# Kernel optimization log

Measured on AMD Instinct MI355X. Metric: run time of the kernel, lower is better.

## Reference

```python
import jax, jax.numpy as jnp
from jax import lax
import numpy as np

BN_EPS = 1e-3


def _bn_train(x, gamma, beta):
    # training-mode BatchNorm2d: batch stats over (N, H, W), biased variance
    mean = jnp.mean(x, axis=(0, 2, 3), keepdims=True)
    var = jnp.var(x, axis=(0, 2, 3), keepdims=True)
    g = gamma[None, :, None, None]
    b = beta[None, :, None, None]
    return (x - mean) * lax.rsqrt(var + BN_EPS) * g + b


def _pointwise(x, w, b, gamma, beta):
    # 1x1 conv + BN + relu (reluM = clamp(min=0))
    y = jnp.einsum('bchw,oc->bohw', x, w) + b[None, :, None, None]
    return jnp.maximum(_bn_train(y, gamma, beta), 0.0)


def _depthwise1d(x, w, b, gamma, beta):
    # depthwise (1,5) conv, zero pad width by 2 each side, BN, clamp(-8,8)
    C = w.shape[0]
    k = w[:, None, None, :]  # [C,1,1,5]
    y = lax.conv_general_dilated(
        x, k, window_strides=(1, 1), padding=[(0, 0), (2, 2)],
        feature_group_count=C,
        dimension_numbers=('NCHW', 'OIHW', 'NCHW'))
    y = y + b[None, :, None, None]
    return jnp.clip(_bn_train(y, gamma, beta), -8.0, 8.0)


def _iir(x, w3, gamma, beta):
    # y[0] = (a+b+c)*x[0];  y[r] = a*x[r] + b*x[r-1] + c*y[r-1]
    a = w3[0][:, None]  # w_curr_inp, [C,1]
    b = w3[1][:, None]  # w_prev_inp
    c = w3[2][:, None]  # w_prev_out
    xT = jnp.moveaxis(x, 2, 0)  # [H,B,C,W]
    y0 = (a + b + c) * xT[0]

    def step(y_prev, xs):
        x_curr, x_prev = xs
        y = a * x_curr + b * x_prev + c * y_prev
        return y, y

    _, ys = lax.scan(step, y0, (xT[1:], xT[:-1]))
    y = jnp.concatenate([y0[None], ys], axis=0)
    y = jnp.moveaxis(y, 0, 2)  # back to [B,C,H,W]
    return jnp.clip(_bn_train(y, gamma, beta), -8.0, 8.0)


def _process_unit(x, u, iir_w, iir_gamma, iir_beta, dw_w, dw_b, dw_gamma,
                  dw_beta, pw_w, pw_b, pw_gamma, pw_beta):
    h = _iir(x, iir_w[u], iir_gamma[u], iir_beta[u])
    h = _depthwise1d(h, dw_w[u], dw_b[u], dw_gamma[u], dw_beta[u])
    return _pointwise(h, pw_w[u], pw_b[u], pw_gamma[u], pw_beta[u])


def setup_inputs() -> dict:
    key = jax.random.key(0)
    ks = jax.random.split(key, 16)
    B, Cin, Cout, H, W = 4, 36, 72, 256, 256
    return {
        'x': jax.random.normal(ks[0], (B, Cin, H, W), jnp.float32),
        'expand_w': jax.random.normal(ks[1], (Cout, Cin), jnp.float32),
        'expand_b': jax.random.normal(ks[2], (Cout,), jnp.float32),
        'expand_gamma': jax.random.uniform(ks[3], (Cout,), jnp.float32),
        'expand_beta': jax.random.normal(ks[4], (Cout,), jnp.float32),
        'iir_w': jax.random.uniform(ks[5], (4, 3, Cout), jnp.float32),
        'iir_gamma': jax.random.uniform(ks[6], (4, Cout), jnp.float32),
        'iir_beta': jax.random.normal(ks[7], (4, Cout), jnp.float32),
        'dw_w': jax.random.normal(ks[8], (4, Cout, 5), jnp.float32),
        'dw_b': jax.random.normal(ks[9], (4, Cout), jnp.float32),
        'dw_gamma': jax.random.uniform(ks[10], (4, Cout), jnp.float32),
        'dw_beta': jax.random.normal(ks[11], (4, Cout), jnp.float32),
        'pw_w': jax.random.normal(ks[12], (4, Cout, Cout), jnp.float32),
        'pw_b': jax.random.normal(ks[13], (4, Cout), jnp.float32),
        'pw_gamma': jax.random.uniform(ks[14], (4, Cout), jnp.float32),
        'pw_beta': jax.random.normal(ks[15], (4, Cout), jnp.float32),
    }


def reference(x, expand_w, expand_b, expand_gamma, expand_beta, iir_w,
              iir_gamma, iir_beta, dw_w, dw_b, dw_gamma, dw_beta, pw_w,
              pw_b, pw_gamma, pw_beta):
    h = _pointwise(x, expand_w, expand_b, expand_gamma, expand_beta)
    unit = lambda z, u: _process_unit(z, u, iir_w, iir_gamma, iir_beta, dw_w,
                                      dw_b, dw_gamma, dw_beta, pw_w, pw_b,
                                      pw_gamma, pw_beta)
    h = h + unit(unit(h, 0), 1)
    h = h + unit(unit(h, 2), 3)
    return h
```

## Files before the change

### kernel.cpp

```cpp
#include <hip/hip_runtime.h>
#include <hip/hip_fp16.h>

#define BBATCH 4
#define CCH 72
#define HROW 256
#define WCOL 256
#define HWSZ (HROW*WCOL)
#define NPC (BBATCH*HROW*WCOL)
#define BNEPS 1e-3f
#define NSH 64
#define SST 144

typedef unsigned short u16;
typedef unsigned int u32;
typedef _Float16 h8 __attribute__((ext_vector_type(8)));
typedef float f32x4 __attribute__((ext_vector_type(4)));

__device__ __forceinline__ float h2f(u16 h_){ return __half2float(__ushort_as_half(h_)); }
__device__ __forceinline__ u16 f2h(float f){ return __half_as_ushort(__float2half(f)); }
__device__ __forceinline__ u32 pack2(float a, float b){ return (u32)f2h(a) | ((u32)f2h(b)<<16); }
__device__ __forceinline__ float clip8(float v){ return fminf(fmaxf(v,-8.f),8.f); }

__device__ __forceinline__ void get_ss_wave(int c, int lane, const float* __restrict__ pstat,
                                            const float* __restrict__ gam, const float* __restrict__ bet,
                                            float& sc, float& sh){
  float s = pstat[lane*SST + c];
  float q = pstat[lane*SST + 72 + c];
  #pragma unroll
  for (int off=32; off; off>>=1){ s += __shfl_xor(s,off); q += __shfl_xor(q,off); }
  float mean = s * (1.0f/(float)NPC);
  float var  = q * (1.0f/(float)NPC) - mean*mean;
  sc = gam[c] * rsqrtf(var + BNEPS);
  sh = bet[c] - mean*sc;
}

template<int CIN, int RAW>
__global__ __launch_bounds__(512) void k_pw(const void* __restrict__ in_,
    u16* __restrict__ out, const float* __restrict__ wgt,
    const float* __restrict__ pstat,
    const float* __restrict__ pgam, const float* __restrict__ pbet,
    float* __restrict__ ostat)
{
  constexpr int KB   = (CIN + 31) / 32;
  constexpr int CPAD = KB * 32;
  constexpr int CST  = CPAD + 1;
  constexpr int XST  = 18;
  constexpr int XSZ  = 16 * CST * XST;
  constexpr int ESZ  = 72 * 264;
  constexpr int SSZ  = (XSZ > ESZ) ? XSZ : ESZ;
  constexpr int NXT  = (CIN*32 + 511) / 512;

  __shared__ u16 W[KB][80][40];
  __shared__ u16 xs[SSZ];
  __shared__ float tsc[80], tsh[80];
  __shared__ float ps2[80], pq2[80];
  __shared__ float sst[72], sqt[72];

  const int tid  = threadIdx.x;
  const int lane = tid & 63;
  const int wid  = tid >> 6;
  const int g    = lane >> 4;
  const int li   = lane & 15;
  const int b    = blockIdx.x >> 8;
  const int hrow = blockIdx.x & 255;

  uint4  xr[NXT];
  float4 xa[NXT], xb[NXT];
  #pragma unroll
  for (int it = 0; it < NXT; ++it){
    int e = tid + it*512;
    if (e < CIN*32){
      int c = e >> 5, o8 = e & 31;
      if constexpr (RAW){
        const float* ip = (const float*)in_ + (size_t)b*CIN*HWSZ + (size_t)c*HWSZ + (size_t)hrow*WCOL + o8*8;
        xa[it] = *(const float4*)ip;
        xb[it] = *(const float4*)(ip+4);
      } else {
        const u16* ip = (const u16*)in_ + (size_t)b*CIN*HWSZ + (size_t)c*HWSZ + (size_t)hrow*WCOL + o8*8;
        xr[it] = *(const uint4*)ip;
      }
    }
  }

  if (tid < 80){ ps2[tid] = 0.f; pq2[tid] = 0.f; }
  if (tid < 72){ sst[tid] = 0.f; sqt[tid] = 0.f; }

  for (int e = tid; e < (CPAD-CIN)*32; e += 512){
    int c = CIN + (e >> 5), o8 = e & 31;
    int pxt = o8 >> 1, pp = (o8 & 1) * 8;
    *(uint4*)&xs[(pxt*CST + c)*XST + pp] = make_uint4(0,0,0,0);
  }

  for (int e = tid; e < KB*80*40; e += 512){
    int kb  = e / 3200;
    int rem = e - kb*3200;
    int row = rem / 40;
    int col = rem - row*40;
    int c   = kb*32 + col;
    float w = 0.f;
    if (row < 72 && col < 32 && c < CIN) w = wgt[row*CIN + c];
    W[kb][row][col] = f2h(w);
  }

  if constexpr (!RAW){
    if ((tid & 127) < 72){
      int c = tid & 127, sg = tid >> 7;
      float s = 0.f, q = 0.f;
      #pragma unroll
      for (int k2 = 0; k2 < 16; ++k2){
        s += pstat[(sg*16 + k2)*SST + c];
        q += pstat[(sg*16 + k2)*SST + 72 + c];
      }
      atomicAdd(&ps2[c], s); atomicAdd(&pq2[c], q);
    }
    __syncthreads();
    if (tid < CIN){
      float mean = ps2[tid] * (1.0f/(float)NPC);
      float var  = pq2[tid] * (1.0f/(float)NPC) - mean*mean;
      float scv  = pgam[tid] * rsqrtf(var + BNEPS);
      tsc[tid] = scv;
      tsh[tid] = pbet[tid] - mean*scv;
    }
  }
  __syncthreads();

  #pragma unroll
  for (int it = 0; it < NXT; ++it){
    int e = tid + it*512;
    if (e < CIN*32){
      int c = e >> 5, o8 = e & 31;
      int pxt = o8 >> 1, pp = (o8 & 1) * 8;
      float v[8];
      if constexpr (RAW){
        v[0]=xa[it].x; v[1]=xa[it].y; v[2]=xa[it].z; v[3]=xa[it].w;
        v[4]=xb[it].x; v[5]=xb[it].y; v[6]=xb[it].z; v[7]=xb[it].w;
      } else {
        u32 rr[4] = {xr[it].x, xr[it].y, xr[it].z, xr[it].w};
        float scv = tsc[c], shv = tsh[c];
        #pragma unroll
        for (int q2=0; q2<4; ++q2){
          v[2*q2]   = clip8(h2f((u16)rr[q2])*scv + shv);
          v[2*q2+1] = clip8(h2f((u16)(rr[q2]>>16))*scv + shv);
        }
      }
      uint4 pk;
      pk.x = pack2(v[0],v[1]); pk.y = pack2(v[2],v[3]);
      pk.z = pack2(v[4],v[5]); pk.w = pack2(v[6],v[7]);
      *(uint4*)&xs[(pxt*CST + c)*XST + pp] = pk;
    }
  }
  __syncthreads();

  f32x4 acc[5][2];
  #pragma unroll
  for (int mt=0; mt<5; ++mt){ acc[mt][0] = (f32x4){0,0,0,0}; acc[mt][1] = (f32x4){0,0,0,0}; }
  const int pxA = wid*2, pxB = wid*2 + 1;
  #pragma unroll
  for (int kb = 0; kb < KB; ++kb){
    h8 bf0, bf1;
    #pragma unroll
    for (int j = 0; j < 8; ++j){
      bf0[j] = *(const _Float16*)&xs[(pxA*CST + kb*32 + g*8 + j)*XST + li];
      bf1[j] = *(const _Float16*)&xs[(pxB*CST + kb*32 + g*8 + j)*XST + li];
    }
    #pragma unroll
    for (int mt = 0; mt < 5; ++mt){
      h8 ah = *(const h8*)&W[kb][mt*16 + li][g*8];
      acc[mt][0] = __builtin_amdgcn_mfma_f32_16x16x32_f16(ah, bf0, acc[mt][0], 0, 0, 0);
      acc[mt][1] = __builtin_amdgcn_mfma_f32_16x16x32_f16(ah, bf1, acc[mt][1], 0, 0, 0);
    }
  }
  __syncthreads();

  #pragma unroll
  for (int mt = 0; mt < 5; ++mt){
    int o = mt*16 + g*4;
    if (o < 72){
      #pragma unroll
      for (int t2 = 0; t2 < 2; ++t2){
        int px = (wid*2 + t2)*16 + li;
        #pragma unroll
        for (int r = 0; r < 4; ++r)
          xs[(o + r)*264 + px] = f2h(acc[mt][t2][r]);
      }
    }
  }
  __syncthreads();

  #pragma unroll
  for (int it = 0; it < 5; ++it){
    int e = tid + it*512;
    if (e < 72*32){
      int o = e >> 5, m = e & 31;
      uint4 v = *(const uint4*)&xs[o*264 + m*8];
      u32 rr[4] = {v.x, v.y, v.z, v.w};
      float s = 0.f, q = 0.f;
      #pragma unroll
      for (int q2=0; q2<4; ++q2){
        float a  = h2f((u16)rr[q2]);
        float bq = h2f((u16)(rr[q2]>>16));
        s += a + bq;
        q = fmaf(a,a,q); q = fmaf(bq,bq,q);
      }
      *(uint4*)(out + (size_t)b*CCH*HWSZ + (size_t)o*HWSZ + (size_t)hrow*WCOL + m*8) = v;
      #pragma unroll
      for (int off = 1; off <= 16; off <<= 1){ s += __shfl_xor(s, off); q += __shfl_xor(q, off); }
      if ((lane & 31) == 0){ atomicAdd(&sst[o], s); atomicAdd(&sqt[o], q); }
    }
  }
  __syncthreads();
  if (tid < 72){
    float* oshard = ostat + (size_t)(blockIdx.x & (NSH-1))*SST;
    atomicAdd(oshard + tid,      sst[tid]);
    atomicAdd(oshard + 72 + tid, sqt[tid]);
  }
}

template<int MODE>
__global__ __launch_bounds__(256) void k_iir(const u16* __restrict__ in, u16* __restrict__ out,
    const float* __restrict__ wabc, u16* __restrict__ hbuf,
    const float* __restrict__ pstat,
    const float* __restrict__ pgam, const float* __restrict__ pbet,
    float* __restrict__ ostat)
{
  const int tid = threadIdx.x;
  const int bc = blockIdx.x;
  const int c = bc % CCH;
  float sc, sh; get_ss_wave(c, tid&63, pstat, pgam, pbet, sc, sh);
  const float ka = wabc[c], kb = wabc[CCH+c], kcc = wabc[2*CCH+c];
  const size_t base = (size_t)bc*HWSZ + tid;
  float xprev=0.f, yprev=0.f, lsum=0.f, lssq=0.f;

  for (int hb = 0; hb < HROW; hb += 16){
    float x[16];
    #pragma unroll
    for (int j=0;j<16;++j){
      size_t idx = base + (size_t)(hb+j)*WCOL;
      float v = fmaxf(h2f(in[idx])*sc + sh, 0.f);
      if (MODE==1) hbuf[idx] = f2h(v);
      if (MODE==2){ v += h2f(hbuf[idx]); hbuf[idx] = f2h(v); }
      x[j] = v;
    }
    if (hb == 0){ xprev = x[0]; yprev = x[0]; }
    float t[16];
    t[0] = fmaf(ka, x[0], kb*xprev);
    #pragma unroll
    for (int j=1;j<16;++j) t[j] = fmaf(ka, x[j], kb*x[j-1]);
    #pragma unroll
    for (int j=0;j<16;++j){
      yprev = fmaf(kcc, yprev, t[j]);
      out[base + (size_t)(hb+j)*WCOL] = f2h(yprev);
      lsum += yprev; lssq = fmaf(yprev,yprev,lssq);
    }
    xprev = x[15];
  }

  #pragma unroll
  for (int off=32; off; off>>=1){ lsum += __shfl_xor(lsum,off); lssq += __shfl_xor(lssq,off); }
  __shared__ float rs[4], rq[4];
  if ((tid&63)==0){ rs[tid>>6]=lsum; rq[tid>>6]=lssq; }
  __syncthreads();
  if (tid==0){
    float* oshard = ostat + (size_t)(blockIdx.x & (NSH-1))*SST;
    atomicAdd(oshard + c,      rs[0]+rs[1]+rs[2]+rs[3]);
    atomicAdd(oshard + 72 + c, rq[0]+rq[1]+rq[2]+rq[3]);
  }
}

__global__ __launch_bounds__(256) void k_dw(const u16* __restrict__ in, u16* __restrict__ out,
    const float* __restrict__ wgt,
    const float* __restrict__ pstat,
    const float* __restrict__ pgam, const float* __restrict__ pbet,
    float* __restrict__ ostat)
{
  __shared__ float xs[8*264];
  __shared__ float rs[4], rq[4];
  const int tid = threadIdx.x;
  const int ht = blockIdx.x & 31;
  const int bc = blockIdx.x >> 5;
  const int c = bc % CCH;
  float sc, sh; get_ss_wave(c, tid&63, pstat, pgam, pbet, sc, sh);
  const float w0=wgt[c*5+0], w1=wgt[c*5+1], w2=wgt[c*5+2], w3=wgt[c*5+3], w4=wgt[c*5+4];
  const size_t base = (size_t)bc*HWSZ + (size_t)ht*(8*WCOL);

  if (tid < 64){
    int r = tid>>3, k = tid&7;
    xs[r*264 + (k<4 ? k : 256+k)] = 0.f;
  }
  const int r = tid >> 5, m = tid & 31;
  {
    uint4 v = *(const uint4*)(in + base + (size_t)r*WCOL + m*8);
    u32 rr[4] = {v.x, v.y, v.z, v.w};
    float f[8];
    #pragma unroll
    for (int q=0;q<4;++q){
      f[2*q]   = clip8(h2f((u16)rr[q])*sc + sh);
      f[2*q+1] = clip8(h2f((u16)(rr[q]>>16))*sc + sh);
    }
    float4* dst = (float4*)&xs[r*264 + 4 + m*8];
    dst[0] = make_float4(f[0],f[1],f[2],f[3]);
    dst[1] = make_float4(f[4],f[5],f[6],f[7]);
  }
  __syncthreads();
  float lsum=0.f, lssq=0.f;
  {
    const float* row = &xs[r*264 + m*8];
    float4 a0 = *(const float4*)(row+0);
    float4 a1 = *(const float4*)(row+4);
    float4 a2 = *(const float4*)(row+8);
    float4 a3 = *(const float4*)(row+12);
    float v[16] = {a0.x,a0.y,a0.z,a0.w, a1.x,a1.y,a1.z,a1.w,
                   a2.x,a2.y,a2.z,a2.w, a3.x,a3.y,a3.z,a3.w};
    float o[8];
    #pragma unroll
    for (int j=0;j<8;++j){
      float y = w0*v[j+2];
      y = fmaf(w1, v[j+3], y);
      y = fmaf(w2, v[j+4], y);
      y = fmaf(w3, v[j+5], y);
      y = fmaf(w4, v[j+6], y);
      o[j] = y;
      lsum += y; lssq = fmaf(y,y,lssq);
    }
    *(uint4*)(out + base + (size_t)r*WCOL + m*8) =
        make_uint4(pack2(o[0],o[1]), pack2(o[2],o[3]), pack2(o[4],o[5]), pack2(o[6],o[7]));
  }
  #pragma unroll
  for (int off=32; off; off>>=1){ lsum += __shfl_xor(lsum,off); lssq += __shfl_xor(lssq,off); }
  if ((tid&63)==0){ rs[tid>>6]=lsum; rq[tid>>6]=lssq; }
  __syncthreads();
  if (tid==0){
    float* oshard = ostat + (size_t)(blockIdx.x & (NSH-1))*SST;
    atomicAdd(oshard + c,      rs[0]+rs[1]+rs[2]+rs[3]);
    atomicAdd(oshard + 72 + c, rq[0]+rq[1]+rq[2]+rq[3]);
  }
}

__global__ __launch_bounds__(256) void k_final(const u16* __restrict__ y12, const u16* __restrict__ h1,
    float* __restrict__ outp,
    const float* __restrict__ pstat,
    const float* __restrict__ pgam, const float* __restrict__ pbet)
{
  __shared__ float tsc[CCH], tsh[CCH];
  if (threadIdx.x < CCH){
    int cc = threadIdx.x;
    float s=0.f, q=0.f;
    for (int sh2=0; sh2<NSH; ++sh2){ s += pstat[sh2*SST + cc]; q += pstat[sh2*SST + 72 + cc]; }
    float mean = s * (1.0f/(float)NPC);
    float var  = q * (1.0f/(float)NPC) - mean*mean;
    float scv = pgam[cc] * rsqrtf(var + BNEPS);
    tsc[cc] = scv;
    tsh[cc] = pbet[cc] - mean*scv;
  }
  __syncthreads();
  const size_t TOTALQ = (size_t)BBATCH*CCH*HWSZ/4;
  for (size_t q = (size_t)blockIdx.x*blockDim.x + threadIdx.x; q < TOTALQ;
       q += (size_t)gridDim.x*blockDim.x){
    int cch = (int)((q >> 14) % CCH);
    float sc = tsc[cch], sh = tsh[cch];
    uint2 a = *(const uint2*)(y12 + q*4);
    uint2 b = *(const uint2*)(h1 + q*4);
    float4 o;
    o.x = fmaxf(h2f((u16)a.x)*sc+sh, 0.f)       + h2f((u16)b.x);
    o.y = fmaxf(h2f((u16)(a.x>>16))*sc+sh, 0.f) + h2f((u16)(b.x>>16));
    o.z = fmaxf(h2f((u16)a.y)*sc+sh, 0.f)       + h2f((u16)b.y);
    o.w = fmaxf(h2f((u16)(a.y>>16))*sc+sh, 0.f) + h2f((u16)(b.y>>16));
    *(float4*)(outp + q*4) = o;
  }
}

extern "C" void kernel_launch(void* const* d_in, const int* in_sizes, int n_in,
                              void* d_out, int out_size, void* d_ws, size_t ws_size,
                              hipStream_t stream)
{
  (void)in_sizes; (void)n_in; (void)out_size;
  const float* x   = (const float*)d_in[0];
  const float* ew  = (const float*)d_in[1];
  const float* eg  = (const float*)d_in[3];
  const float* ebt = (const float*)d_in[4];
  const float* iw  = (const float*)d_in[5];
  const float* ig  = (const float*)d_in[6];
  const float* ibt = (const float*)d_in[7];
  const float* dwt = (const float*)d_in[8];
  const float* dg  = (const float*)d_in[10];
  const float* dbt = (const float*)d_in[11];
  const float* pw  = (const float*)d_in[12];
  const float* pg  = (const float*)d_in[14];
  const float* pbt = (const float*)d_in[15];
  float* outp = (float*)d_out;

  const size_t BUFE = (size_t)BBATCH*CCH*HWSZ;
  const size_t BUFB = BUFE*2;
  const size_t STATSB = (size_t)13*NSH*SST*sizeof(float);
  char* ws = (char*)d_ws;
  u16* A = (u16*)ws;
  u16* H = (u16*)(ws + BUFB);
  u16* B;
  float* stats;
  if (ws_size >= 3*BUFB + STATSB + 256){
    B = (u16*)(ws + 2*BUFB);
    stats = (float*)(ws + 3*BUFB);
  } else {
    B = (u16*)d_out;
    stats = (float*)(ws + 2*BUFB);
  }
  #define ST(s) (stats + (size_t)(s)*NSH*SST)

  hipMemsetAsync(stats, 0, STATSB, stream);

  dim3 blk(256);
  dim3 blkpw(512);
  k_pw<36,1><<<BBATCH*HROW, blkpw, 0, stream>>>((const void*)x, A, ew,
      nullptr, nullptr, nullptr, ST(0));
  k_iir<1><<<BBATCH*CCH, blk, 0, stream>>>(A, B, iw+0,   H, ST(0), eg, ebt, ST(1));
  k_dw    <<<BBATCH*CCH*32, blk, 0, stream>>>(B, A, dwt+0,    ST(1), ig+0,   ibt+0,   ST(2));
  k_pw<72,0><<<BBATCH*HROW, blkpw, 0, stream>>>(A, B, pw+0,     ST(2), dg+0,   dbt+0,   ST(3));
  k_iir<0><<<BBATCH*CCH, blk, 0, stream>>>(B, A, iw+216, nullptr, ST(3), pg+0,  pbt+0,  ST(4));
  k_dw    <<<BBATCH*CCH*32, blk, 0, stream>>>(A, B, dwt+360,  ST(4), ig+72,  ibt+72,  ST(5));
  k_pw<72,0><<<BBATCH*HROW, blkpw, 0, stream>>>(B, A, pw+5184,  ST(5), dg+72,  dbt+72,  ST(6));
  k_iir<2><<<BBATCH*CCH, blk, 0, stream>>>(A, B, iw+432, H, ST(6), pg+72, pbt+72, ST(7));
  k_dw    <<<BBATCH*CCH*32, blk, 0, stream>>>(B, A, dwt+720,  ST(7), ig+144, ibt+144, ST(8));
  k_pw<72,0><<<BBATCH*HROW, blkpw, 0, stream>>>(A, B, pw+10368, ST(8), dg+144, dbt+144, ST(9));
  k_iir<0><<<BBATCH*CCH, blk, 0, stream>>>(B, A, iw+648, nullptr, ST(9), pg+144, pbt+144, ST(10));
  k_dw    <<<BBATCH*CCH*32, blk, 0, stream>>>(A, B, dwt+1080, ST(10), ig+216, ibt+216, ST(11));
  k_pw<72,0><<<BBATCH*HROW, blkpw, 0, stream>>>(B, A, pw+15552, ST(11), dg+216, dbt+216, ST(12));
  k_final<<<2048, blk, 0, stream>>>(A, H, outp, ST(12), pg+216, pbt+216);
  #undef ST
}
```

Baseline: 377.3 us.

## Pre-pack fp16 weights once, read from global, and double-buffer IIR loads

```diff
diff --git a/kernel.cpp b/kernel.cpp
--- a/kernel.cpp
+++ b/kernel.cpp
@@ -34,9 +34,28 @@
   sh = bet[c] - mean*sc;
 }
 
+__global__ __launch_bounds__(256) void k_prep(const float* __restrict__ ew,
+    const float* __restrict__ pwall, u16* __restrict__ Wp)
+{
+  for (int e = blockIdx.x*256 + threadIdx.x; e < 14*3200; e += gridDim.x*256){
+    int slab = e / 3200, rem = e - slab*3200;
+    int row = rem / 40, col = rem - row*40;
+    float w = 0.f;
+    if (slab < 2){
+      int c = slab*32 + col;
+      if (row < 72 && col < 32 && c < 36) w = ew[row*36 + c];
+    } else {
+      int u = (slab-2)/3, kb = (slab-2)%3;
+      int c = kb*32 + col;
+      if (row < 72 && col < 32) w = pwall[u*5184 + row*72 + c];
+    }
+    Wp[e] = f2h(w);
+  }
+}
+
 template<int CIN, int RAW>
 __global__ __launch_bounds__(512) void k_pw(const void* __restrict__ in_,
-    u16* __restrict__ out, const float* __restrict__ wgt,
+    u16* __restrict__ out, const u16* __restrict__ Wp,
     const float* __restrict__ pstat,
     const float* __restrict__ pgam, const float* __restrict__ pbet,
     float* __restrict__ ostat)
@@ -50,10 +69,9 @@
   constexpr int SSZ  = (XSZ > ESZ) ? XSZ : ESZ;
   constexpr int NXT  = (CIN*32 + 511) / 512;
 
-  __shared__ u16 W[KB][80][40];
   __shared__ u16 xs[SSZ];
   __shared__ float tsc[80], tsh[80];
-  __shared__ float ps2[80], pq2[80];
+  __shared__ float pp4[4][72], pq4[4][72];
   __shared__ float sst[72], sqt[72];
 
   const int tid  = threadIdx.x;
@@ -82,7 +100,6 @@
     }
   }
 
-  if (tid < 80){ ps2[tid] = 0.f; pq2[tid] = 0.f; }
   if (tid < 72){ sst[tid] = 0.f; sqt[tid] = 0.f; }
 
   for (int e = tid; e < (CPAD-CIN)*32; e += 512){
@@ -91,32 +108,23 @@
     *(uint4*)&xs[(pxt*CST + c)*XST + pp] = make_uint4(0,0,0,0);
   }
 
-  for (int e = tid; e < KB*80*40; e += 512){
-    int kb  = e / 3200;
-    int rem = e - kb*3200;
-    int row = rem / 40;
-    int col = rem - row*40;
-    int c   = kb*32 + col;
-    float w = 0.f;
-    if (row < 72 && col < 32 && c < CIN) w = wgt[row*CIN + c];
-    W[kb][row][col] = f2h(w);
-  }
-
   if constexpr (!RAW){
-    if ((tid & 127) < 72){
-      int c = tid & 127, sg = tid >> 7;
+    int sg = tid >> 7, c = tid & 127;
+    if (c < 72){
       float s = 0.f, q = 0.f;
       #pragma unroll
       for (int k2 = 0; k2 < 16; ++k2){
         s += pstat[(sg*16 + k2)*SST + c];
         q += pstat[(sg*16 + k2)*SST + 72 + c];
       }
-      atomicAdd(&ps2[c], s); atomicAdd(&pq2[c], q);
+      pp4[sg][c] = s; pq4[sg][c] = q;
     }
     __syncthreads();
     if (tid < CIN){
-      float mean = ps2[tid] * (1.0f/(float)NPC);
-      float var  = pq2[tid] * (1.0f/(float)NPC) - mean*mean;
+      float s = pp4[0][tid] + pp4[1][tid] + pp4[2][tid] + pp4[3][tid];
+      float q = pq4[0][tid] + pq4[1][tid] + pq4[2][tid] + pq4[3][tid];
+      float mean = s * (1.0f/(float)NPC);
+      float var  = q * (1.0f/(float)NPC) - mean*mean;
       float scv  = pgam[tid] * rsqrtf(var + BNEPS);
       tsc[tid] = scv;
       tsh[tid] = pbet[tid] - mean*scv;
@@ -165,7 +173,7 @@
     }
     #pragma unroll
     for (int mt = 0; mt < 5; ++mt){
-      h8 ah = *(const h8*)&W[kb][mt*16 + li][g*8];
+      h8 ah = *(const h8*)(Wp + (size_t)(kb*80 + mt*16 + li)*40 + g*8);
       acc[mt][0] = __builtin_amdgcn_mfma_f32_16x16x32_f16(ah, bf0, acc[mt][0], 0, 0, 0);
       acc[mt][1] = __builtin_amdgcn_mfma_f32_16x16x32_f16(ah, bf1, acc[mt][1], 0, 0, 0);
     }
@@ -231,14 +239,23 @@
   const size_t base = (size_t)bc*HWSZ + tid;
   float xprev=0.f, yprev=0.f, lsum=0.f, lssq=0.f;
 
-  for (int hb = 0; hb < HROW; hb += 16){
-    float x[16];
+  float a0[16], a1[16], r0[16], r1[16];
+
+  auto LOADC = [&](int hb, float* xv, float* rv){
     #pragma unroll
     for (int j=0;j<16;++j){
       size_t idx = base + (size_t)(hb+j)*WCOL;
-      float v = fmaxf(h2f(in[idx])*sc + sh, 0.f);
-      if (MODE==1) hbuf[idx] = f2h(v);
-      if (MODE==2){ v += h2f(hbuf[idx]); hbuf[idx] = f2h(v); }
+      xv[j] = h2f(in[idx]);
+      if (MODE==2) rv[j] = h2f(hbuf[idx]);
+    }
+  };
+  auto COMPC = [&](int hb, const float* xv, const float* rv){
+    float x[16];
+    #pragma unroll
+    for (int j=0;j<16;++j){
+      float v = fmaxf(xv[j]*sc + sh, 0.f);
+      if (MODE==1) hbuf[base + (size_t)(hb+j)*WCOL] = f2h(v);
+      if (MODE==2){ v += rv[j]; hbuf[base + (size_t)(hb+j)*WCOL] = f2h(v); }
       x[j] = v;
     }
     if (hb == 0){ xprev = x[0]; yprev = x[0]; }
@@ -253,6 +270,15 @@
       lsum += yprev; lssq = fmaf(yprev,yprev,lssq);
     }
     xprev = x[15];
+  };
+
+  LOADC(0, a0, r0);
+  #pragma unroll
+  for (int hb = 0; hb < HROW; hb += 32){
+    LOADC(hb+16, a1, r1);
+    COMPC(hb, a0, r0);
+    if (hb+32 < HROW) LOADC(hb+32, a0, r0);
+    COMPC(hb+16, a1, r1);
   }
 
   #pragma unroll
@@ -392,38 +418,43 @@
   const size_t BUFE = (size_t)BBATCH*CCH*HWSZ;
   const size_t BUFB = BUFE*2;
   const size_t STATSB = (size_t)13*NSH*SST*sizeof(float);
+  const size_t WPB = (size_t)14*3200*sizeof(u16);
   char* ws = (char*)d_ws;
   u16* A = (u16*)ws;
   u16* H = (u16*)(ws + BUFB);
   u16* B;
   float* stats;
-  if (ws_size >= 3*BUFB + STATSB + 256){
+  if (ws_size >= 3*BUFB + STATSB + WPB + 256){
     B = (u16*)(ws + 2*BUFB);
     stats = (float*)(ws + 3*BUFB);
   } else {
     B = (u16*)d_out;
     stats = (float*)(ws + 2*BUFB);
   }
+  u16* Wp = (u16*)((char*)stats + STATSB);
   #define ST(s) (stats + (size_t)(s)*NSH*SST)
+  #define WSLAB(u) (Wp + (size_t)(2 + 3*(u))*3200)
 
   hipMemsetAsync(stats, 0, STATSB, stream);
 
   dim3 blk(256);
   dim3 blkpw(512);
-  k_pw<36,1><<<BBATCH*HROW, blkpw, 0, stream>>>((const void*)x, A, ew,
+  k_prep<<<18, blk, 0, stream>>>(ew, pw, Wp);
+  k_pw<36,1><<<BBATCH*HROW, blkpw, 0, stream>>>((const void*)x, A, Wp,
       nullptr, nullptr, nullptr, ST(0));
   k_iir<1><<<BBATCH*CCH, blk, 0, stream>>>(A, B, iw+0,   H, ST(0), eg, ebt, ST(1));
   k_dw    <<<BBATCH*CCH*32, blk, 0, stream>>>(B, A, dwt+0,    ST(1), ig+0,   ibt+0,   ST(2));
-  k_pw<72,0><<<BBATCH*HROW, blkpw, 0, stream>>>(A, B, pw+0,     ST(2), dg+0,   dbt+0,   ST(3));
+  k_pw<72,0><<<BBATCH*HROW, blkpw, 0, stream>>>(A, B, WSLAB(0), ST(2), dg+0,   dbt+0,   ST(3));
   k_iir<0><<<BBATCH*CCH, blk, 0, stream>>>(B, A, iw+216, nullptr, ST(3), pg+0,  pbt+0,  ST(4));
   k_dw    <<<BBATCH*CCH*32, blk, 0, stream>>>(A, B, dwt+360,  ST(4), ig+72,  ibt+72,  ST(5));
-  k_pw<72,0><<<BBATCH*HROW, blkpw, 0, stream>>>(B, A, pw+5184,  ST(5), dg+72,  dbt+72,  ST(6));
+  k_pw<72,0><<<BBATCH*HROW, blkpw, 0, stream>>>(B, A, WSLAB(1), ST(5), dg+72,  dbt+72,  ST(6));
   k_iir<2><<<BBATCH*CCH, blk, 0, stream>>>(A, B, iw+432, H, ST(6), pg+72, pbt+72, ST(7));
   k_dw    <<<BBATCH*CCH*32, blk, 0, stream>>>(B, A, dwt+720,  ST(7), ig+144, ibt+144, ST(8));
-  k_pw<72,0><<<BBATCH*HROW, blkpw, 0, stream>>>(A, B, pw+10368, ST(8), dg+144, dbt+144, ST(9));
+  k_pw<72,0><<<BBATCH*HROW, blkpw, 0, stream>>>(A, B, WSLAB(2), ST(8), dg+144, dbt+144, ST(9));
   k_iir<0><<<BBATCH*CCH, blk, 0, stream>>>(B, A, iw+648, nullptr, ST(9), pg+144, pbt+144, ST(10));
   k_dw    <<<BBATCH*CCH*32, blk, 0, stream>>>(A, B, dwt+1080, ST(10), ig+216, ibt+216, ST(11));
-  k_pw<72,0><<<BBATCH*HROW, blkpw, 0, stream>>>(B, A, pw+15552, ST(11), dg+216, dbt+216, ST(12));
+  k_pw<72,0><<<BBATCH*HROW, blkpw, 0, stream>>>(B, A, WSLAB(3), ST(11), dg+216, dbt+216, ST(12));
   k_final<<<2048, blk, 0, stream>>>(A, H, outp, ST(12), pg+216, pbt+216);
   #undef ST
-}
+  #undef WSLAB
+}
```

Result: faster. 339.2 us (-10.1%).
